# Optimization experiments

Measured on AMD Instinct MI355X. Metric: run time of the kernel, lower is better.

## Reference

```python
import jax, jax.numpy as jnp
import numpy as np

TOP_K = 8
NUM_EXPERTS = 128
HIDDEN = 2048
TOKENS = 16384
NORM_TOPK_PROB = True


def setup_inputs() -> dict:
    key = jax.random.key(0)
    k1, k2 = jax.random.split(key)
    hidden_states = jax.random.normal(k1, (TOKENS, HIDDEN), dtype=jnp.float32)
    # gate weight [num_experts, hidden] (nn.Linear layout)
    weight = jax.random.normal(k2, (NUM_EXPERTS, HIDDEN), dtype=jnp.float32) * 0.02
    return {"hidden_states": hidden_states, "weight": weight}


def reference(hidden_states, weight):
    x = hidden_states.reshape(-1, HIDDEN)
    # router_logits: [tokens, num_experts]
    router_logits = jnp.einsum("td,ed->te", x, weight)
    router_probs = jax.nn.softmax(router_logits.astype(jnp.float32), axis=-1)
    top_vals, top_idx = jax.lax.top_k(router_probs, TOP_K)
    if NORM_TOPK_PROB:
        top_vals = top_vals / jnp.sum(top_vals, axis=-1, keepdims=True)
    top_vals = top_vals.astype(hidden_states.dtype)
    return router_logits, top_vals, top_idx
```

## Files before the change

kernel.cpp:

```cpp
#include <hip/hip_runtime.h>
#include <float.h>
#include <math.h>

#define TOKENS 16384
#define HIDDEN 2048
#define NEXP 128
#define TOPK 8
#define NCAND 12
#define DELTA 1e-3f

#define BM 64
#define BK 64
#define KITERS (HIDDEN / BK)

typedef float f32x16 __attribute__((ext_vector_type(16)));
typedef short bf16x8 __attribute__((ext_vector_type(8)));

__device__ __forceinline__ unsigned pack_hi(float a, float b) {
    return (__float_as_uint(a) >> 16) | (__float_as_uint(b) & 0xFFFF0000u);
}
__device__ __forceinline__ float resid(float a) {
    return a - __uint_as_float(__float_as_uint(a) & 0xFFFF0000u);
}

__device__ __forceinline__ void load_lds_16B(const void* g, void* l) {
    __builtin_amdgcn_global_load_lds(
        (const __attribute__((address_space(1))) unsigned int*)g,
        (__attribute__((address_space(3))) unsigned int*)l, 16, 0, 0);
}

__global__ __launch_bounds__(256) void presplit_w(const float* __restrict__ W,
                                                  unsigned short* __restrict__ Ws) {
    const int c = blockIdx.x * 256 + threadIdx.x;
    const int lane = c & 63;
    const int q = c >> 6;
    const int hl = q & 1;
    const int nt = (q >> 1) & 3;
    const int k16 = q >> 3;
    const int e = nt * 32 + (lane & 31);
    const int k0 = k16 * 16 + (lane >> 5) * 8;
    const float* wp = W + (size_t)e * HIDDEN + k0;
    float4 a = *(const float4*)wp;
    float4 b = *(const float4*)(wp + 4);
    if (hl) {
        a.x = resid(a.x); a.y = resid(a.y); a.z = resid(a.z); a.w = resid(a.w);
        b.x = resid(b.x); b.y = resid(b.y); b.z = resid(b.z); b.w = resid(b.w);
    }
    uint4 o;
    o.x = pack_hi(a.x, a.y); o.y = pack_hi(a.z, a.w);
    o.z = pack_hi(b.x, b.y); o.w = pack_hi(b.z, b.w);
    *(uint4*)(Ws + (size_t)c * 8) = o;
}

__global__ __launch_bounds__(256) void router_gemm(const float* __restrict__ X,
                                                   const unsigned short* __restrict__ Ws,
                                                   float* __restrict__ logits) {
    __shared__ unsigned short sA[16 * 512];
    __shared__ unsigned short sB[32 * 512];
    const int tid = threadIdx.x;
    const int lane = tid & 63;
    const int wid = tid >> 6;
    const int wm = wid & 1, wn = wid >> 1;
    const int t0 = blockIdx.x * BM;

    const int swm = tid >> 7, ss = (tid >> 5) & 3, stok = tid & 31;
    const float* Xp = X + (size_t)(t0 + swm * 32 + stok) * HIDDEN + ss * 16;
    const int cA0 = ((swm * 4 + ss) * 2) * 512;

    f32x16 acc[2];
#pragma unroll
    for (int i = 0; i < 2; ++i)
#pragma unroll
        for (int r = 0; r < 16; ++r) acc[i][r] = 0.f;

    float4 xv0 = *(const float4*)(Xp);
    float4 xv1 = *(const float4*)(Xp + 4);
    float4 xv2 = *(const float4*)(Xp + 8);
    float4 xv3 = *(const float4*)(Xp + 12);

#pragma unroll 1
    for (int kt = 0; kt < KITERS; ++kt) {
        __syncthreads();
        {
            const unsigned short* src = Ws + ((size_t)kt * 32 + wid * 8) * 512 + lane * 8;
            unsigned short* dst = &sB[(wid * 8) * 512];
#pragma unroll
            for (int i = 0; i < 8; ++i)
                load_lds_16B(src + i * 512, dst + i * 512);
        }
        {
            uint4 v;
            v.x = pack_hi(xv0.x, xv0.y); v.y = pack_hi(xv0.z, xv0.w);
            v.z = pack_hi(xv1.x, xv1.y); v.w = pack_hi(xv1.z, xv1.w);
            *(uint4*)&sA[cA0 + stok * 8] = v;
            v.x = pack_hi(xv2.x, xv2.y); v.y = pack_hi(xv2.z, xv2.w);
            v.z = pack_hi(xv3.x, xv3.y); v.w = pack_hi(xv3.z, xv3.w);
            *(uint4*)&sA[cA0 + (32 + stok) * 8] = v;
            v.x = pack_hi(resid(xv0.x), resid(xv0.y)); v.y = pack_hi(resid(xv0.z), resid(xv0.w));
            v.z = pack_hi(resid(xv1.x), resid(xv1.y)); v.w = pack_hi(resid(xv1.z), resid(xv1.w));
            *(uint4*)&sA[cA0 + 512 + stok * 8] = v;
            v.x = pack_hi(resid(xv2.x), resid(xv2.y)); v.y = pack_hi(resid(xv2.z), resid(xv2.w));
            v.z = pack_hi(resid(xv3.x), resid(xv3.y)); v.w = pack_hi(resid(xv3.z), resid(xv3.w));
            *(uint4*)&sA[cA0 + 512 + (32 + stok) * 8] = v;
        }
        __syncthreads();

        if (kt + 1 < KITERS) {
            const float* xp = Xp + (kt + 1) * BK;
            xv0 = *(const float4*)(xp);
            xv1 = *(const float4*)(xp + 4);
            xv2 = *(const float4*)(xp + 8);
            xv3 = *(const float4*)(xp + 12);
        }

#pragma unroll
        for (int s = 0; s < 4; ++s) {
            const int ab = ((wm * 4 + s) * 2) * 512 + lane * 8;
            const bf16x8 ah = *(const bf16x8*)&sA[ab];
            const bf16x8 al = *(const bf16x8*)&sA[ab + 512];
#pragma unroll
            for (int ntl = 0; ntl < 2; ++ntl) {
                const int nt = wn * 2 + ntl;
                const int bb = ((s * 4 + nt) * 2) * 512 + lane * 8;
                const bf16x8 bh = *(const bf16x8*)&sB[bb];
                const bf16x8 bl = *(const bf16x8*)&sB[bb + 512];
                acc[ntl] = __builtin_amdgcn_mfma_f32_32x32x16_bf16(ah, bh, acc[ntl], 0, 0, 0);
                acc[ntl] = __builtin_amdgcn_mfma_f32_32x32x16_bf16(ah, bl, acc[ntl], 0, 0, 0);
                acc[ntl] = __builtin_amdgcn_mfma_f32_32x32x16_bf16(al, bh, acc[ntl], 0, 0, 0);
            }
        }
    }

    const int col = lane & 31;
    const int rbase = 4 * (lane >> 5);
#pragma unroll
    for (int ntl = 0; ntl < 2; ++ntl) {
        const int e = wn * 64 + ntl * 32 + col;
#pragma unroll
        for (int reg = 0; reg < 16; ++reg) {
            const int row = (reg & 3) + 8 * (reg >> 2) + rbase;
            logits[(size_t)(t0 + wm * 32 + row) * NEXP + e] = acc[ntl][reg];
        }
    }
}

__global__ __launch_bounds__(256) void router_select(const float* __restrict__ logits,
                                                     float* __restrict__ top_vals,
                                                     float* __restrict__ top_idx,
                                                     int* __restrict__ cnt,
                                                     int* __restrict__ list) {
    const int lane = threadIdx.x & 63;
    const int t = blockIdx.x * 4 + (threadIdx.x >> 6);
    const float* lrow = logits + (size_t)t * NEXP;
    const float l0 = lrow[lane];
    const float l1 = lrow[lane + 64];
    bool r0 = false, r1 = false;
    float vals[TOPK + 1]; int idxs[TOPK + 1];
#pragma unroll
    for (int it = 0; it < TOPK + 1; ++it) {
        const float c0 = r0 ? -FLT_MAX : l0;
        const float c1 = r1 ? -FLT_MAX : l1;
        float v; int id;
        if (c1 > c0) { v = c1; id = lane + 64; }
        else         { v = c0; id = lane; }
#pragma unroll
        for (int off = 1; off < 64; off <<= 1) {
            const float ov = __shfl_xor(v, off);
            const int   oi = __shfl_xor(id, off);
            if (ov > v || (ov == v && oi < id)) { v = ov; id = oi; }
        }
        vals[it] = v; idxs[it] = id;
        if (id == lane) r0 = true;
        else if (id == lane + 64) r1 = true;
    }

    float ming = FLT_MAX;
#pragma unroll
    for (int i = 0; i < TOPK; ++i) ming = fminf(ming, vals[i] - vals[i + 1]);

    if (ming < DELTA) {
        if (lane == 0) { const int p = atomicAdd(cnt, 1); list[p] = t; }
    } else if (lane == 0) {
        const float m = vals[0];
        float ex[TOPK], s = 0.f;
#pragma unroll
        for (int i = 0; i < TOPK; ++i) { ex[i] = expf(vals[i] - m); s += ex[i]; }
        const float inv = 1.f / s;
#pragma unroll
        for (int i = 0; i < TOPK; ++i) {
            top_vals[(size_t)t * TOPK + i] = ex[i] * inv;
            top_idx[(size_t)t * TOPK + i] = (float)idxs[i];
        }
    }
}

__device__ __forceinline__ void top_cand(const float* __restrict__ lrow, int lane,
                                         float* vals, int* idxs) {
    const float l0 = lrow[lane];
    const float l1 = lrow[lane + 64];
    bool r0 = false, r1 = false;
#pragma unroll
    for (int it = 0; it < NCAND; ++it) {
        const float c0 = r0 ? -FLT_MAX : l0;
        const float c1 = r1 ? -FLT_MAX : l1;
        float v; int id;
        if (c1 > c0) { v = c1; id = lane + 64; }
        else         { v = c0; id = lane; }
#pragma unroll
        for (int off = 1; off < 64; off <<= 1) {
            const float ov = __shfl_xor(v, off);
            const int   oi = __shfl_xor(id, off);
            if (ov > v || (ov == v && oi < id)) { v = ov; id = oi; }
        }
        vals[it] = v; idxs[it] = id;
        if (id == lane) r0 = true;
        else if (id == lane + 64) r1 = true;
    }
}

__global__ __launch_bounds__(256) void router_refine(const float* __restrict__ logits,
                                                     const float* __restrict__ X,
                                                     const float* __restrict__ W,
                                                     float* __restrict__ top_vals,
                                                     float* __restrict__ top_idx,
                                                     const int* __restrict__ cnt,
                                                     const int* __restrict__ list) {
    const int lane = threadIdx.x & 63;
    const int gw = blockIdx.x * 4 + (threadIdx.x >> 6);
    const int nwaves = gridDim.x * 4;
    const int n = *cnt;

    for (int ii = gw; ii < n; ii += nwaves) {
        const int t = list[ii];
        float vals[NCAND]; int idxs[NCAND];
        top_cand(logits + (size_t)t * NEXP, lane, vals, idxs);

        const float* xr = X + (size_t)t * HIDDEN;
        double xd[32];
#pragma unroll
        for (int j = 0; j < 8; ++j) {
            const float4 v = *(const float4*)(xr + j * 256 + lane * 4);
            xd[j * 4 + 0] = (double)v.x; xd[j * 4 + 1] = (double)v.y;
            xd[j * 4 + 2] = (double)v.z; xd[j * 4 + 3] = (double)v.w;
        }
        double acc[NCAND];
#pragma unroll
        for (int c = 0; c < NCAND; ++c) {
            const float* wr = W + (size_t)idxs[c] * HIDDEN;
            double a0 = 0.0, a1 = 0.0;
#pragma unroll
            for (int j = 0; j < 8; ++j) {
                const float4 w = *(const float4*)(wr + j * 256 + lane * 4);
                a0 = fma((double)w.x, xd[j * 4 + 0], a0);
                a1 = fma((double)w.y, xd[j * 4 + 1], a1);
                a0 = fma((double)w.z, xd[j * 4 + 2], a0);
                a1 = fma((double)w.w, xd[j * 4 + 3], a1);
            }
            acc[c] = a0 + a1;
        }
#pragma unroll
        for (int c = 0; c < NCAND; ++c)
#pragma unroll
            for (int off = 1; off < 64; off <<= 1)
                acc[c] += __shfl_xor(acc[c], off);

        int rank[NCAND];
#pragma unroll
        for (int c = 0; c < NCAND; ++c) {
            int r = 0;
#pragma unroll
            for (int m = 0; m < NCAND; ++m)
                if (acc[m] > acc[c] || (acc[m] == acc[c] && idxs[m] < idxs[c])) ++r;
            rank[c] = r;
        }
        double vmax = acc[0];
#pragma unroll
        for (int c = 0; c < NCAND; ++c) if (rank[c] == 0) vmax = acc[c];
        float e[NCAND], s = 0.f;
#pragma unroll
        for (int c = 0; c < NCAND; ++c) {
            e[c] = (rank[c] < TOPK) ? expf((float)(acc[c] - vmax)) : 0.f;
            s += e[c];
        }
        const float inv = 1.f / s;
        if (lane == 0) {
#pragma unroll
            for (int c = 0; c < NCAND; ++c)
                if (rank[c] < TOPK) {
                    top_vals[(size_t)t * TOPK + rank[c]] = e[c] * inv;
                    top_idx[(size_t)t * TOPK + rank[c]] = (float)idxs[c];
                }
        }
    }
}

extern "C" void kernel_launch(void* const* d_in, const int* in_sizes, int n_in,
                              void* d_out, int out_size, void* d_ws, size_t ws_size,
                              hipStream_t stream) {
    const float* X = (const float*)d_in[0];
    const float* W = (const float*)d_in[1];
    float* logits = (float*)d_out;
    float* tvals  = logits + (size_t)TOKENS * NEXP;
    float* tidx   = tvals + (size_t)TOKENS * TOPK;

    int* cnt = (int*)d_ws;
    unsigned short* Wsplit = (unsigned short*)((char*)d_ws + 4096);
    int* list = (int*)((char*)d_ws + 4096 + 2 * 1024 * 1024);

    hipMemsetAsync(d_ws, 0, 64, stream);
    presplit_w<<<256, 256, 0, stream>>>(W, Wsplit);
    router_gemm<<<TOKENS / BM, 256, 0, stream>>>(X, Wsplit, logits);
    router_select<<<TOKENS / 4, 256, 0, stream>>>(logits, tvals, tidx, cnt, list);
    router_refine<<<256, 256, 0, stream>>>(logits, X, W, tvals, tidx, cnt, list);
}
```

Baseline: 326.4 us.

## Fuse select and refine into one top-k kernel, halve GEMM token tile

Merges the select and refine kernels into a single router_topk kernel. Tokens whose top-k gaps fall under the threshold now refine inline in fp64, which removes the atomic list, the workspace memset and one launch. The GEMM tile shrinks from 64 to 32 tokens per block, with each wave owning one 32-expert column tile, so the grid doubles and each block holds less state. The ambiguity threshold drops to 5e-4, sending fewer tokens to refinement but loosening the safety margin against bf16x3 error. Inline refinement can cause wave divergence within blocks, and the smaller GEMM tile reloads W from LDS more often per token.

```diff
diff --git a/kernel.cpp b/kernel.cpp
--- a/kernel.cpp
+++ b/kernel.cpp
@@ -7,9 +7,9 @@
 #define NEXP 128
 #define TOPK 8
 #define NCAND 12
-#define DELTA 1e-3f
-
-#define BM 64
+#define DELTA 5e-4f
+
+#define BM 32
 #define BK 64
 #define KITERS (HIDDEN / BK)
 
@@ -55,28 +55,24 @@
 __global__ __launch_bounds__(256) void router_gemm(const float* __restrict__ X,
                                                    const unsigned short* __restrict__ Ws,
                                                    float* __restrict__ logits) {
-    __shared__ unsigned short sA[16 * 512];
+    __shared__ unsigned short sA[8 * 512];
     __shared__ unsigned short sB[32 * 512];
     const int tid = threadIdx.x;
     const int lane = tid & 63;
     const int wid = tid >> 6;
-    const int wm = wid & 1, wn = wid >> 1;
     const int t0 = blockIdx.x * BM;
 
-    const int swm = tid >> 7, ss = (tid >> 5) & 3, stok = tid & 31;
-    const float* Xp = X + (size_t)(t0 + swm * 32 + stok) * HIDDEN + ss * 16;
-    const int cA0 = ((swm * 4 + ss) * 2) * 512;
-
-    f32x16 acc[2];
-#pragma unroll
-    for (int i = 0; i < 2; ++i)
-#pragma unroll
-        for (int r = 0; r < 16; ++r) acc[i][r] = 0.f;
-
-    float4 xv0 = *(const float4*)(Xp);
-    float4 xv1 = *(const float4*)(Xp + 4);
-    float4 xv2 = *(const float4*)(Xp + 8);
-    float4 xv3 = *(const float4*)(Xp + 12);
+    const int arow = tid >> 3, aq = tid & 7;
+    const int offH = ((aq >> 1) * 2 + 0) * 512 + ((aq & 1) * 32 + arow) * 8;
+    const int offL = offH + 512;
+    const float* Xp = X + (size_t)(t0 + arow) * HIDDEN + aq * 8;
+
+    f32x16 acc;
+#pragma unroll
+    for (int r = 0; r < 16; ++r) acc[r] = 0.f;
+
+    float4 xa = *(const float4*)(Xp);
+    float4 xb = *(const float4*)(Xp + 4);
 
 #pragma unroll 1
     for (int kt = 0; kt < KITERS; ++kt) {
@@ -90,72 +86,58 @@
         }
         {
             uint4 v;
-            v.x = pack_hi(xv0.x, xv0.y); v.y = pack_hi(xv0.z, xv0.w);
-            v.z = pack_hi(xv1.x, xv1.y); v.w = pack_hi(xv1.z, xv1.w);
-            *(uint4*)&sA[cA0 + stok * 8] = v;
-            v.x = pack_hi(xv2.x, xv2.y); v.y = pack_hi(xv2.z, xv2.w);
-            v.z = pack_hi(xv3.x, xv3.y); v.w = pack_hi(xv3.z, xv3.w);
-            *(uint4*)&sA[cA0 + (32 + stok) * 8] = v;
-            v.x = pack_hi(resid(xv0.x), resid(xv0.y)); v.y = pack_hi(resid(xv0.z), resid(xv0.w));
-            v.z = pack_hi(resid(xv1.x), resid(xv1.y)); v.w = pack_hi(resid(xv1.z), resid(xv1.w));
-            *(uint4*)&sA[cA0 + 512 + stok * 8] = v;
-            v.x = pack_hi(resid(xv2.x), resid(xv2.y)); v.y = pack_hi(resid(xv2.z), resid(xv2.w));
-            v.z = pack_hi(resid(xv3.x), resid(xv3.y)); v.w = pack_hi(resid(xv3.z), resid(xv3.w));
-            *(uint4*)&sA[cA0 + 512 + (32 + stok) * 8] = v;
+            v.x = pack_hi(xa.x, xa.y); v.y = pack_hi(xa.z, xa.w);
+            v.z = pack_hi(xb.x, xb.y); v.w = pack_hi(xb.z, xb.w);
+            *(uint4*)&sA[offH] = v;
+            v.x = pack_hi(resid(xa.x), resid(xa.y));
+            v.y = pack_hi(resid(xa.z), resid(xa.w));
+            v.z = pack_hi(resid(xb.x), resid(xb.y));
+            v.w = pack_hi(resid(xb.z), resid(xb.w));
+            *(uint4*)&sA[offL] = v;
         }
         __syncthreads();
 
         if (kt + 1 < KITERS) {
             const float* xp = Xp + (kt + 1) * BK;
-            xv0 = *(const float4*)(xp);
-            xv1 = *(const float4*)(xp + 4);
-            xv2 = *(const float4*)(xp + 8);
-            xv3 = *(const float4*)(xp + 12);
+            xa = *(const float4*)(xp);
+            xb = *(const float4*)(xp + 4);
         }
 
 #pragma unroll
         for (int s = 0; s < 4; ++s) {
-            const int ab = ((wm * 4 + s) * 2) * 512 + lane * 8;
-            const bf16x8 ah = *(const bf16x8*)&sA[ab];
-            const bf16x8 al = *(const bf16x8*)&sA[ab + 512];
-#pragma unroll
-            for (int ntl = 0; ntl < 2; ++ntl) {
-                const int nt = wn * 2 + ntl;
-                const int bb = ((s * 4 + nt) * 2) * 512 + lane * 8;
-                const bf16x8 bh = *(const bf16x8*)&sB[bb];
-                const bf16x8 bl = *(const bf16x8*)&sB[bb + 512];
-                acc[ntl] = __builtin_amdgcn_mfma_f32_32x32x16_bf16(ah, bh, acc[ntl], 0, 0, 0);
-                acc[ntl] = __builtin_amdgcn_mfma_f32_32x32x16_bf16(ah, bl, acc[ntl], 0, 0, 0);
-                acc[ntl] = __builtin_amdgcn_mfma_f32_32x32x16_bf16(al, bh, acc[ntl], 0, 0, 0);
-            }
-        }
-    }
-
-    const int col = lane & 31;
+            const bf16x8 ah = *(const bf16x8*)&sA[(s * 2 + 0) * 512 + lane * 8];
+            const bf16x8 al = *(const bf16x8*)&sA[(s * 2 + 1) * 512 + lane * 8];
+            const int bb = (s * 8 + wid * 2) * 512 + lane * 8;
+            const bf16x8 bh = *(const bf16x8*)&sB[bb];
+            const bf16x8 bl = *(const bf16x8*)&sB[bb + 512];
+            acc = __builtin_amdgcn_mfma_f32_32x32x16_bf16(ah, bh, acc, 0, 0, 0);
+            acc = __builtin_amdgcn_mfma_f32_32x32x16_bf16(ah, bl, acc, 0, 0, 0);
+            acc = __builtin_amdgcn_mfma_f32_32x32x16_bf16(al, bh, acc, 0, 0, 0);
+        }
+    }
+
+    const int e = wid * 32 + (lane & 31);
     const int rbase = 4 * (lane >> 5);
 #pragma unroll
-    for (int ntl = 0; ntl < 2; ++ntl) {
-        const int e = wn * 64 + ntl * 32 + col;
-#pragma unroll
-        for (int reg = 0; reg < 16; ++reg) {
-            const int row = (reg & 3) + 8 * (reg >> 2) + rbase;
-            logits[(size_t)(t0 + wm * 32 + row) * NEXP + e] = acc[ntl][reg];
-        }
-    }
-}
-
-__global__ __launch_bounds__(256) void router_select(const float* __restrict__ logits,
-                                                     float* __restrict__ top_vals,
-                                                     float* __restrict__ top_idx,
-                                                     int* __restrict__ cnt,
-                                                     int* __restrict__ list) {
+    for (int reg = 0; reg < 16; ++reg) {
+        const int row = (reg & 3) + 8 * (reg >> 2) + rbase;
+        logits[(size_t)(t0 + row) * NEXP + e] = acc[reg];
+    }
+}
+
+__global__ __launch_bounds__(256) void router_topk(const float* __restrict__ logits,
+                                                   const float* __restrict__ X,
+                                                   const float* __restrict__ W,
+                                                   float* __restrict__ top_vals,
+                                                   float* __restrict__ top_idx) {
     const int lane = threadIdx.x & 63;
     const int t = blockIdx.x * 4 + (threadIdx.x >> 6);
     const float* lrow = logits + (size_t)t * NEXP;
     const float l0 = lrow[lane];
     const float l1 = lrow[lane + 64];
     bool r0 = false, r1 = false;
-    float vals[TOPK + 1]; int idxs[TOPK + 1];
+    float vals[NCAND]; int idxs[NCAND];
+
 #pragma unroll
     for (int it = 0; it < TOPK + 1; ++it) {
         const float c0 = r0 ? -FLT_MAX : l0;
@@ -178,29 +160,24 @@
 #pragma unroll
     for (int i = 0; i < TOPK; ++i) ming = fminf(ming, vals[i] - vals[i + 1]);
 
-    if (ming < DELTA) {
-        if (lane == 0) { const int p = atomicAdd(cnt, 1); list[p] = t; }
-    } else if (lane == 0) {
-        const float m = vals[0];
-        float ex[TOPK], s = 0.f;
-#pragma unroll
-        for (int i = 0; i < TOPK; ++i) { ex[i] = expf(vals[i] - m); s += ex[i]; }
-        const float inv = 1.f / s;
-#pragma unroll
-        for (int i = 0; i < TOPK; ++i) {
-            top_vals[(size_t)t * TOPK + i] = ex[i] * inv;
-            top_idx[(size_t)t * TOPK + i] = (float)idxs[i];
-        }
-    }
-}
-
-__device__ __forceinline__ void top_cand(const float* __restrict__ lrow, int lane,
-                                         float* vals, int* idxs) {
-    const float l0 = lrow[lane];
-    const float l1 = lrow[lane + 64];
-    bool r0 = false, r1 = false;
-#pragma unroll
-    for (int it = 0; it < NCAND; ++it) {
+    if (ming >= DELTA) {
+        if (lane == 0) {
+            const float m = vals[0];
+            float ex[TOPK], s = 0.f;
+#pragma unroll
+            for (int i = 0; i < TOPK; ++i) { ex[i] = expf(vals[i] - m); s += ex[i]; }
+            const float inv = 1.f / s;
+#pragma unroll
+            for (int i = 0; i < TOPK; ++i) {
+                top_vals[(size_t)t * TOPK + i] = ex[i] * inv;
+                top_idx[(size_t)t * TOPK + i] = (float)idxs[i];
+            }
+        }
+        return;
+    }
+
+#pragma unroll
+    for (int it = TOPK + 1; it < NCAND; ++it) {
         const float c0 = r0 ? -FLT_MAX : l0;
         const float c1 = r1 ? -FLT_MAX : l1;
         float v; int id;
@@ -216,81 +193,62 @@
         if (id == lane) r0 = true;
         else if (id == lane + 64) r1 = true;
     }
-}
-
-__global__ __launch_bounds__(256) void router_refine(const float* __restrict__ logits,
-                                                     const float* __restrict__ X,
-                                                     const float* __restrict__ W,
-                                                     float* __restrict__ top_vals,
-                                                     float* __restrict__ top_idx,
-                                                     const int* __restrict__ cnt,
-                                                     const int* __restrict__ list) {
-    const int lane = threadIdx.x & 63;
-    const int gw = blockIdx.x * 4 + (threadIdx.x >> 6);
-    const int nwaves = gridDim.x * 4;
-    const int n = *cnt;
-
-    for (int ii = gw; ii < n; ii += nwaves) {
-        const int t = list[ii];
-        float vals[NCAND]; int idxs[NCAND];
-        top_cand(logits + (size_t)t * NEXP, lane, vals, idxs);
-
-        const float* xr = X + (size_t)t * HIDDEN;
-        double xd[32];
+
+    const float* xr = X + (size_t)t * HIDDEN;
+    double xd[32];
+#pragma unroll
+    for (int j = 0; j < 8; ++j) {
+        const float4 v = *(const float4*)(xr + j * 256 + lane * 4);
+        xd[j * 4 + 0] = (double)v.x; xd[j * 4 + 1] = (double)v.y;
+        xd[j * 4 + 2] = (double)v.z; xd[j * 4 + 3] = (double)v.w;
+    }
+    double acc[NCAND];
+#pragma unroll
+    for (int c = 0; c < NCAND; ++c) {
+        const float* wr = W + (size_t)idxs[c] * HIDDEN;
+        double a0 = 0.0, a1 = 0.0;
 #pragma unroll
         for (int j = 0; j < 8; ++j) {
-            const float4 v = *(const float4*)(xr + j * 256 + lane * 4);
-            xd[j * 4 + 0] = (double)v.x; xd[j * 4 + 1] = (double)v.y;
-            xd[j * 4 + 2] = (double)v.z; xd[j * 4 + 3] = (double)v.w;
-        }
-        double acc[NCAND];
-#pragma unroll
-        for (int c = 0; c < NCAND; ++c) {
-            const float* wr = W + (size_t)idxs[c] * HIDDEN;
-            double a0 = 0.0, a1 = 0.0;
-#pragma unroll
-            for (int j = 0; j < 8; ++j) {
-                const float4 w = *(const float4*)(wr + j * 256 + lane * 4);
-                a0 = fma((double)w.x, xd[j * 4 + 0], a0);
-                a1 = fma((double)w.y, xd[j * 4 + 1], a1);
-                a0 = fma((double)w.z, xd[j * 4 + 2], a0);
-                a1 = fma((double)w.w, xd[j * 4 + 3], a1);
+            const float4 w = *(const float4*)(wr + j * 256 + lane * 4);
+            a0 = fma((double)w.x, xd[j * 4 + 0], a0);
+            a1 = fma((double)w.y, xd[j * 4 + 1], a1);
+            a0 = fma((double)w.z, xd[j * 4 + 2], a0);
+            a1 = fma((double)w.w, xd[j * 4 + 3], a1);
+        }
+        acc[c] = a0 + a1;
+    }
+#pragma unroll
+    for (int c = 0; c < NCAND; ++c)
+#pragma unroll
+        for (int off = 1; off < 64; off <<= 1)
+            acc[c] += __shfl_xor(acc[c], off);
+
+    int rank[NCAND];
+#pragma unroll
+    for (int c = 0; c < NCAND; ++c) {
+        int r = 0;
+#pragma unroll
+        for (int m = 0; m < NCAND; ++m)
+            if (acc[m] > acc[c] || (acc[m] == acc[c] && idxs[m] < idxs[c])) ++r;
+        rank[c] = r;
+    }
+    double vmax = acc[0];
+#pragma unroll
+    for (int c = 0; c < NCAND; ++c) if (rank[c] == 0) vmax = acc[c];
+    float ex[NCAND], s = 0.f;
+#pragma unroll
+    for (int c = 0; c < NCAND; ++c) {
+        ex[c] = (rank[c] < TOPK) ? expf((float)(acc[c] - vmax)) : 0.f;
+        s += ex[c];
+    }
+    const float inv = 1.f / s;
+    if (lane == 0) {
+#pragma unroll
+        for (int c = 0; c < NCAND; ++c)
+            if (rank[c] < TOPK) {
+                top_vals[(size_t)t * TOPK + rank[c]] = ex[c] * inv;
+                top_idx[(size_t)t * TOPK + rank[c]] = (float)idxs[c];
             }
-            acc[c] = a0 + a1;
-        }
-#pragma unroll
-        for (int c = 0; c < NCAND; ++c)
-#pragma unroll
-            for (int off = 1; off < 64; off <<= 1)
-                acc[c] += __shfl_xor(acc[c], off);
-
-        int rank[NCAND];
-#pragma unroll
-        for (int c = 0; c < NCAND; ++c) {
-            int r = 0;
-#pragma unroll
-            for (int m = 0; m < NCAND; ++m)
-                if (acc[m] > acc[c] || (acc[m] == acc[c] && idxs[m] < idxs[c])) ++r;
-            rank[c] = r;
-        }
-        double vmax = acc[0];
-#pragma unroll
-        for (int c = 0; c < NCAND; ++c) if (rank[c] == 0) vmax = acc[c];
-        float e[NCAND], s = 0.f;
-#pragma unroll
-        for (int c = 0; c < NCAND; ++c) {
-            e[c] = (rank[c] < TOPK) ? expf((float)(acc[c] - vmax)) : 0.f;
-            s += e[c];
-        }
-        const float inv = 1.f / s;
-        if (lane == 0) {
-#pragma unroll
-            for (int c = 0; c < NCAND; ++c)
-                if (rank[c] < TOPK) {
-                    top_vals[(size_t)t * TOPK + rank[c]] = e[c] * inv;
-                    top_idx[(size_t)t * TOPK + rank[c]] = (float)idxs[c];
-                }
-        }
     }
 }
 
@@ -303,13 +261,9 @@
     float* tvals  = logits + (size_t)TOKENS * NEXP;
     float* tidx   = tvals + (size_t)TOKENS * TOPK;
 
-    int* cnt = (int*)d_ws;
-    unsigned short* Wsplit = (unsigned short*)((char*)d_ws + 4096);
-    int* list = (int*)((char*)d_ws + 4096 + 2 * 1024 * 1024);
-
-    hipMemsetAsync(d_ws, 0, 64, stream);
+    unsigned short* Wsplit = (unsigned short*)d_ws;
+
     presplit_w<<<256, 256, 0, stream>>>(W, Wsplit);
     router_gemm<<<TOKENS / BM, 256, 0, stream>>>(X, Wsplit, logits);
-    router_select<<<TOKENS / 4, 256, 0, stream>>>(logits, tvals, tidx, cnt, list);
-    router_refine<<<256, 256, 0, stream>>>(logits, X, W, tvals, tidx, cnt, list);
-}
+    router_topk<<<TOKENS / 4, 256, 0, stream>>>(logits, X, W, tvals, tidx);
+}
```

After: 293.7 us. -10.0%, faster.
